# Kernel optimization log

Hardware: AMD Instinct MI355X
Metric: run time of the kernel (lower is better)

Reference implementation:

```python
import jax, jax.numpy as jnp
import numpy as np
import math

D_MODEL = 2048
N_HEADS = 16
HEAD_DIM = 128
ROPE_THETA = 10000.0


def apply_rope(x, pos, theta=ROPE_THETA):
    # x: [b, h, s, d], pos: [b, s] int
    d = x.shape[-1]
    inv_freq = 1.0 / (theta ** (jnp.arange(0, d, 2, dtype=jnp.float32) / d))  # [d/2]
    ang = pos.astype(jnp.float32)[:, None, :, None] * inv_freq  # [b,1,s,d/2]
    cos, sin = jnp.cos(ang), jnp.sin(ang)
    x1, x2 = x[..., 0::2], x[..., 1::2]
    out_even = x1 * cos - x2 * sin
    out_odd = x1 * sin + x2 * cos
    return jnp.stack([out_even, out_odd], axis=-1).reshape(x.shape)


def setup_inputs() -> dict:
    key = jax.random.key(0)
    ks = jax.random.split(key, 5)
    b, s = 2, 2048
    scale = 1.0 / math.sqrt(D_MODEL)
    x = jax.random.normal(ks[0], (b, s, D_MODEL), dtype=jnp.float32)
    Wq = jax.random.normal(ks[1], (D_MODEL, D_MODEL), dtype=jnp.float32) * scale
    Wk = jax.random.normal(ks[2], (D_MODEL, D_MODEL), dtype=jnp.float32) * scale
    Wv = jax.random.normal(ks[3], (D_MODEL, D_MODEL), dtype=jnp.float32) * scale
    Wo = jax.random.normal(ks[4], (D_MODEL, D_MODEL), dtype=jnp.float32) * scale
    token_positions = jnp.broadcast_to(jnp.arange(s, dtype=jnp.int32), (b, s))
    return {"x": x, "token_positions": token_positions, "Wq": Wq, "Wk": Wk, "Wv": Wv, "Wo": Wo}


def reference(x, token_positions, Wq, Wk, Wv, Wo):
    b, s, _ = x.shape
    h, d = N_HEADS, HEAD_DIM
    # QKV projections (Linear: x @ W.T), split heads: b s (h d) -> b h s d
    def proj(W):
        y = jnp.einsum('bse,fe->bsf', x, W)
        return y.reshape(b, s, h, d).transpose(0, 2, 1, 3)
    Q, K, V = proj(Wq), proj(Wk), proj(Wv)
    Q = apply_rope(Q, token_positions)
    K = apply_rope(K, token_positions)
    logits = jnp.einsum('bhqd,bhkd->bhqk', Q, K) / math.sqrt(d)
    causal = jnp.triu(jnp.ones((s, s), dtype=bool), 1)
    logits = jnp.where(causal, -jnp.inf, logits)
    attn = jax.nn.softmax(logits, axis=-1)
    ctx = jnp.einsum('bhqk,bhkd->bhqd', attn, V)
    ctx = ctx.transpose(0, 2, 1, 3).reshape(b, s, h * d)
    return jnp.einsum('bsf,ef->bse', ctx, Wo)
```

## Files before the change

### kernel.cpp

```cpp
#include <hip/hip_runtime.h>
#include <cstdint>
#include <cstddef>

typedef __bf16 bf16_t;
typedef __bf16 bf16x8 __attribute__((ext_vector_type(8)));
typedef float  f32x4  __attribute__((ext_vector_type(4)));

#define SEQ 2048
#define NH  16
#define HD  128
#define MM  4096
#define KK  2048

#define ASYNC16(g, l) __builtin_amdgcn_global_load_lds( \
    (const __attribute__((address_space(1))) void*)(g), \
    (__attribute__((address_space(3))) void*)(l), 16, 0, 0)

__global__ __launch_bounds__(256) void cast_all(const float* __restrict__ x,
                                                const float* __restrict__ Wq,
                                                const float* __restrict__ Wk,
                                                const float* __restrict__ Wv,
                                                const float* __restrict__ Wo,
                                                bf16_t* __restrict__ xb,
                                                bf16_t* __restrict__ wqkv,
                                                bf16_t* __restrict__ wob) {
    int i = blockIdx.x * 256 + threadIdx.x;
    const float* src;
    bf16_t* dst;
    int off;
    if (i < 2097152) { src = x; dst = xb; off = i; }
    else {
        int j = i - 2097152;
        int sel = j >> 20; off = j & 0xFFFFF;
        if (sel < 3) { src = (sel == 0) ? Wq : (sel == 1) ? Wk : Wv; dst = wqkv + (size_t)sel * 4194304; }
        else         { src = Wo; dst = wob; }
    }
    float4 v = ((const float4*)src)[off];
    union { bf16_t h[4]; uint2 u; } t;
    t.h[0] = (bf16_t)v.x; t.h[1] = (bf16_t)v.y;
    t.h[2] = (bf16_t)v.z; t.h[3] = (bf16_t)v.w;
    ((uint2*)dst)[off] = t.u;
}

union SMemU {
    struct { bf16_t A[2][4096]; bf16_t B[2][4096]; } st;
    bf16_t epi[64 * 136];
};

template<int MODE>
__device__ __forceinline__ void gemm_body(SMemU& sm,
                                          const bf16_t* __restrict__ A,
                                          const bf16_t* __restrict__ B,
                                          void* __restrict__ Cout,
                                          bf16_t* __restrict__ Kout,
                                          bf16_t* __restrict__ Vout,
                                          const int* __restrict__ pos) {
    const int tid = threadIdx.x;
    const int w = tid >> 6, l = tid & 63;
    const int lane16 = l & 15, quad = l >> 4;
    const int tm = blockIdx.y, tn = blockIdx.x;
    const int wm = w >> 1, wn = w & 1;

    const bf16_t* pA0 = A + (size_t)(tm * 128 + (2 * w + 0) * 16 + lane16) * KK + quad * 8;
    const bf16_t* pA1 = A + (size_t)(tm * 128 + (2 * w + 1) * 16 + lane16) * KK + quad * 8;
    const bf16_t* pB0 = B + (size_t)(tn * 128 + (2 * w + 0) * 16 + lane16) * KK + quad * 8;
    const bf16_t* pB1 = B + (size_t)(tn * 128 + (2 * w + 1) * 16 + lane16) * KK + quad * 8;

    bf16_t* wA0_0 = &sm.st.A[0][(2 * w + 0) * 512];
    bf16_t* wA1_0 = &sm.st.A[0][(2 * w + 1) * 512];
    bf16_t* wA0_1 = &sm.st.A[1][(2 * w + 0) * 512];
    bf16_t* wA1_1 = &sm.st.A[1][(2 * w + 1) * 512];
    bf16_t* wB0_0 = &sm.st.B[0][(2 * w + 0) * 512];
    bf16_t* wB1_0 = &sm.st.B[0][(2 * w + 1) * 512];
    bf16_t* wB0_1 = &sm.st.B[1][(2 * w + 0) * 512];
    bf16_t* wB1_1 = &sm.st.B[1][(2 * w + 1) * 512];

    f32x4 acc[4][4];
    for (int i = 0; i < 4; i++)
        for (int j = 0; j < 4; j++) acc[i][j] = (f32x4){0.f, 0.f, 0.f, 0.f};

    for (int k0 = 0; k0 < KK; k0 += 64) {
        __syncthreads();
        ASYNC16(pA0, wA0_0); ASYNC16(pA1, wA1_0);
        ASYNC16(pB0, wB0_0); ASYNC16(pB1, wB1_0);
        ASYNC16(pA0 + 32, wA0_1); ASYNC16(pA1 + 32, wA1_1);
        ASYNC16(pB0 + 32, wB0_1); ASYNC16(pB1 + 32, wB1_1);
        pA0 += 64; pA1 += 64; pB0 += 64; pB1 += 64;
        __syncthreads();
        #pragma unroll
        for (int kh = 0; kh < 2; kh++) {
            const bf16_t* rA = &sm.st.A[kh][wm * 2048 + l * 8];
            const bf16_t* rB = &sm.st.B[kh][wn * 2048 + l * 8];
            bf16x8 af[4], bfr[4];
            for (int i = 0; i < 4; i++) af[i]  = *(const bf16x8*)(rA + i * 512);
            for (int j = 0; j < 4; j++) bfr[j] = *(const bf16x8*)(rB + j * 512);
            for (int i = 0; i < 4; i++)
                for (int j = 0; j < 4; j++)
                    acc[i][j] = __builtin_amdgcn_mfma_f32_16x16x32_bf16(af[i], bfr[j], acc[i][j], 0, 0, 0);
        }
    }

    if (MODE == 1) {
        const int mbase = tm * 128 + wm * 64;
        const int nbase = tn * 128 + wn * 64;
        for (int i = 0; i < 4; i++)
            for (int j = 0; j < 4; j++) {
                const int n  = nbase + j * 16 + lane16;
                const int m0 = mbase + i * 16 + quad * 4;
                for (int r = 0; r < 4; r++)
                    ((float*)Cout)[(size_t)(m0 + r) * 2048 + n] = acc[i][j][r];
            }
        return;
    }

    const int mbase = tm * 128;
    const int nb    = tn * 128;
    const int sel   = nb >> 11;
    const int hh    = (nb & 2047) >> 7;
    const int bidx  = mbase >> 11;
    const int g  = tid >> 4;
    const int c8 = (tid & 15) * 8;

    if (sel < 2) {
        bf16_t* dstbase = ((sel == 0) ? (bf16_t*)Cout : Kout) +
                          (size_t)(bidx * NH + hh) * SEQ * HD;
        const float qs = (sel == 0) ? 0.08838834764831845f : 1.0f;
        for (int half = 0; half < 2; half++) {
            __syncthreads();
            if (wm == half) {
                for (int i = 0; i < 4; i++)
                    for (int j = 0; j < 4; j++)
                        for (int r = 0; r < 4; r++)
                            sm.epi[(i * 16 + quad * 4 + r) * 136 + wn * 64 + j * 16 + lane16] =
                                (bf16_t)acc[i][j][r];
            }
            __syncthreads();
            for (int p = 0; p < 4; p++) {
                const int rid = p * 16 + g;
                const int s = (mbase & 2047) + half * 64 + rid;
                bf16x8 v = *(const bf16x8*)&sm.epi[rid * 136 + c8];
                const float pp = (float)pos[bidx * SEQ + s];
                union { bf16_t h8[8]; uint4 u; } o;
                for (int t = 0; t < 4; t++) {
                    const int fi = (c8 >> 1) + t;
                    const float freq = exp2f(-(float)fi * 0.20762050593045857f);
                    const float ang = pp * freq;
                    const float sn = __sinf(ang), cs = __cosf(ang);
                    const float x1 = (float)v[2 * t], x2 = (float)v[2 * t + 1];
                    o.h8[2 * t]     = (bf16_t)((x1 * cs - x2 * sn) * qs);
                    o.h8[2 * t + 1] = (bf16_t)((x1 * sn + x2 * cs) * qs);
                }
                *(uint4*)(dstbase + (size_t)s * HD + c8) = o.u;
            }
        }
    } else {
        bf16_t* dstb = Vout + (size_t)(bidx * NH + hh) * HD * SEQ;
        const int s0 = mbase & 2047;
        for (int half = 0; half < 2; half++) {
            __syncthreads();
            if (wn == half) {
                for (int i = 0; i < 4; i++)
                    for (int j = 0; j < 4; j++) {
                        union { bf16_t h4[4]; uint2 u; } pk;
                        for (int r = 0; r < 4; r++) pk.h4[r] = (bf16_t)acc[i][j][r];
                        *(uint2*)&sm.epi[(j * 16 + lane16) * 136 + wm * 64 + i * 16 + quad * 4] = pk.u;
                    }
            }
            __syncthreads();
            for (int p = 0; p < 4; p++) {
                const int rid = p * 16 + g;
                const int d = half * 64 + rid;
                bf16x8 v = *(const bf16x8*)&sm.epi[rid * 136 + c8];
                *(uint4*)(dstb + (size_t)d * SEQ + s0 + c8) = *(const uint4*)&v;
            }
        }
    }
}

__global__ __launch_bounds__(256) void gemm_qkv(const bf16_t* __restrict__ A,
                                                const bf16_t* __restrict__ B,
                                                bf16_t* __restrict__ Qout,
                                                bf16_t* __restrict__ Kout,
                                                bf16_t* __restrict__ Vout,
                                                const int* __restrict__ pos) {
    __shared__ SMemU sm;
    gemm_body<3>(sm, A, B, (void*)Qout, Kout, Vout, pos);
}

__global__ __launch_bounds__(256) void gemm_out(const bf16_t* __restrict__ A,
                                                const bf16_t* __restrict__ B,
                                                float* __restrict__ Cout) {
    __shared__ SMemU sm;
    gemm_body<1>(sm, A, B, (void*)Cout, nullptr, nullptr, nullptr);
}

__global__ __launch_bounds__(256) void attn_kernel(const bf16_t* __restrict__ Q,
                                                   const bf16_t* __restrict__ K,
                                                   const bf16_t* __restrict__ Vt,
                                                   bf16_t* __restrict__ ctx) {
    const int flat = blockIdx.x;
    const int bh = flat & 31;
    const int bt = flat >> 5;
    const int h = bh & 15, b = bh >> 4;
    const bf16_t* Qh = Q  + (size_t)bh * SEQ * HD;
    const bf16_t* Kh = K  + (size_t)bh * SEQ * HD;
    const bf16_t* Vh = Vt + (size_t)bh * HD * SEQ;

    const int tid = threadIdx.x;
    const int w = tid >> 6, l = tid & 63;
    const int lane16 = l & 15, quad = l >> 4;

    __shared__ bf16_t kt[2][16 * 512];
    __shared__ bf16_t vt[2][16 * 512];
    __shared__ bf16_t pbuf[4][1024];

    for (int half = 0; half < 2; half++) {
        const int qt = half ? (31 - bt) : bt;
        const int q0 = qt * 64 + w * 16;

        bf16x8 qf[4];
        {
            const bf16_t* qrow = Qh + (size_t)(q0 + lane16) * HD + quad * 8;
            for (int kc = 0; kc < 4; kc++) qf[kc] = *(const bf16x8*)(qrow + kc * 32);
        }

        f32x4 o[8];
        for (int dt = 0; dt < 8; dt++) o[dt] = (f32x4){0.f, 0.f, 0.f, 0.f};
        float m_s = -INFINITY, l_s = 0.f;

        __syncthreads();
        for (int ii = 0; ii < 4; ii++) {
            const int f = w * 4 + ii;
            const int nt = f >> 2, kc = f & 3;
            ASYNC16(Kh + (size_t)(nt * 16 + lane16) * HD + kc * 32 + quad * 8, &kt[0][f * 512]);
            const int dt = f >> 1, kk = f & 1;
            ASYNC16(Vh + (size_t)(dt * 16 + lane16) * SEQ + kk * 32 + quad * 8, &vt[0][f * 512]);
        }

        int cur = 0;
        for (int kb = 0; kb <= qt; kb++) {
            const int k0 = kb * 64;
            __syncthreads();
            if (kb < qt) {
                const int kn = k0 + 64;
                for (int ii = 0; ii < 4; ii++) {
                    const int f = w * 4 + ii;
                    const int nt = f >> 2, kc = f & 3;
                    ASYNC16(Kh + (size_t)(kn + nt * 16 + lane16) * HD + kc * 32 + quad * 8,
                            &kt[1 - cur][f * 512]);
                    const int dt = f >> 1, kk = f & 1;
                    ASYNC16(Vh + (size_t)(dt * 16 + lane16) * SEQ + kn + kk * 32 + quad * 8,
                            &vt[1 - cur][f * 512]);
                }
            }
            const bf16_t* ktc = kt[cur];
            const bf16_t* vtc = vt[cur];

            f32x4 sacc[4];
            for (int nt = 0; nt < 4; nt++) sacc[nt] = (f32x4){0.f, 0.f, 0.f, 0.f};
            for (int nt = 0; nt < 4; nt++)
                for (int kc = 0; kc < 4; kc++) {
                    bf16x8 kf = *(const bf16x8*)&ktc[(nt * 4 + kc) * 512 + l * 8];
                    sacc[nt] = __builtin_amdgcn_mfma_f32_16x16x32_bf16(kf, qf[kc], sacc[nt], 0, 0, 0);
                }
            if (kb == qt) {
                const int qg = q0 + lane16;
                for (int nt = 0; nt < 4; nt++)
                    for (int r = 0; r < 4; r++) {
                        const int kg = k0 + nt * 16 + quad * 4 + r;
                        if (kg > qg) sacc[nt][r] = -INFINITY;
                    }
            }
            float rowmax = sacc[0][0];
            for (int nt = 0; nt < 4; nt++)
                for (int r = 0; r < 4; r++) rowmax = fmaxf(rowmax, sacc[nt][r]);
            rowmax = fmaxf(rowmax, __shfl_xor(rowmax, 16, 64));
            rowmax = fmaxf(rowmax, __shfl_xor(rowmax, 32, 64));
            const float mnew = fmaxf(m_s, rowmax);
            const float a = __expf(m_s - mnew);
            m_s = mnew;
            float ssum = 0.f;
            for (int nt = 0; nt < 4; nt++) {
                union { bf16_t h4[4]; uint2 u; } pk;
                for (int r = 0; r < 4; r++) {
                    const float e = __expf(sacc[nt][r] - mnew);
                    ssum += e;
                    pk.h4[r] = (bf16_t)e;
                }
                const int addr = (nt >> 1) * 512 +
                                 (((nt & 1) * 2 + (quad >> 1)) * 16 + lane16) * 8 +
                                 (quad & 1) * 4;
                *(uint2*)&pbuf[w][addr] = pk.u;
            }
            ssum += __shfl_xor(ssum, 16, 64);
            ssum += __shfl_xor(ssum, 32, 64);
            l_s = l_s * a + ssum;

            float ar[4];
            for (int r = 0; r < 4; r++) ar[r] = __shfl(a, (quad << 2) | r, 16);
            for (int dt = 0; dt < 8; dt++)
                for (int r = 0; r < 4; r++) o[dt][r] *= ar[r];
            for (int kk = 0; kk < 2; kk++) {
                bf16x8 pf = *(const bf16x8*)&pbuf[w][kk * 512 + l * 8];
                for (int dt = 0; dt < 8; dt++) {
                    bf16x8 vf = *(const bf16x8*)&vtc[(dt * 2 + kk) * 512 + l * 8];
                    o[dt] = __builtin_amdgcn_mfma_f32_16x16x32_bf16(pf, vf, o[dt], 0, 0, 0);
                }
            }
            cur ^= 1;
        }

        float inv[4];
        for (int r = 0; r < 4; r++) inv[r] = 1.0f / __shfl(l_s, (quad << 2) | r, 16);
        for (int r = 0; r < 4; r++) {
            const int qg = q0 + quad * 4 + r;
            bf16_t* dst = ctx + ((size_t)(b * SEQ + qg)) * (NH * HD) + h * HD;
            for (int dt = 0; dt < 8; dt++)
                dst[dt * 16 + lane16] = (bf16_t)(o[dt][r] * inv[r]);
        }
        __syncthreads();
    }
}

extern "C" void kernel_launch(void* const* d_in, const int* in_sizes, int n_in,
                              void* d_out, int out_size, void* d_ws, size_t ws_size,
                              hipStream_t stream) {
    const float* x  = (const float*)d_in[0];
    const int* pos  = (const int*)d_in[1];
    const float* Wq = (const float*)d_in[2];
    const float* Wk = (const float*)d_in[3];
    const float* Wv = (const float*)d_in[4];
    const float* Wo = (const float*)d_in[5];

    char* ws = (char*)d_ws;
    bf16_t* xb   = (bf16_t*)(ws);
    bf16_t* wqkv = (bf16_t*)(ws + (16u << 20));
    bf16_t* wob  = (bf16_t*)(ws + (40u << 20));
    bf16_t* Qb   = (bf16_t*)(ws + (48u << 20));
    bf16_t* Kb   = (bf16_t*)(ws + (64u << 20));
    bf16_t* Vt   = (bf16_t*)(ws + (80u << 20));
    bf16_t* ctx  = (bf16_t*)(ws + (96u << 20));

    cast_all<<<24576, 256, 0, stream>>>(x, Wq, Wk, Wv, Wo, xb, wqkv, wob);

    dim3 gq(6144 / 128, MM / 128);
    gemm_qkv<<<gq, 256, 0, stream>>>(xb, wqkv, Qb, Kb, Vt, pos);

    attn_kernel<<<512, 256, 0, stream>>>(Qb, Kb, Vt, ctx);

    dim3 gg(2048 / 128, MM / 128);
    gemm_out<<<gg, 256, 0, stream>>>(ctx, wob, (float*)d_out);
}
```

Baseline: 462.3 us.

## Double-buffer GEMM K-loop with async LDS prefetch of next tile

Restructures the projection GEMM main loop to issue async global-to-LDS loads for the next 32-wide K slice into the alternate buffer, then compute MFMAs on the current one. Previously each iteration loaded both halves of a 64-wide slice and waited before computing, so memory and math never overlapped. The loop now runs one barrier per 32-wide step, the same barrier count per K element as before. The gain depends on whether the compiler puts a full vmcnt wait before the LDS reads, which would serialize the prefetch again.

```diff
diff --git a/kernel.cpp b/kernel.cpp
--- a/kernel.cpp
+++ b/kernel.cpp
@@ -66,38 +66,35 @@
     const bf16_t* pB0 = B + (size_t)(tn * 128 + (2 * w + 0) * 16 + lane16) * KK + quad * 8;
     const bf16_t* pB1 = B + (size_t)(tn * 128 + (2 * w + 1) * 16 + lane16) * KK + quad * 8;
 
-    bf16_t* wA0_0 = &sm.st.A[0][(2 * w + 0) * 512];
-    bf16_t* wA1_0 = &sm.st.A[0][(2 * w + 1) * 512];
-    bf16_t* wA0_1 = &sm.st.A[1][(2 * w + 0) * 512];
-    bf16_t* wA1_1 = &sm.st.A[1][(2 * w + 1) * 512];
-    bf16_t* wB0_0 = &sm.st.B[0][(2 * w + 0) * 512];
-    bf16_t* wB1_0 = &sm.st.B[0][(2 * w + 1) * 512];
-    bf16_t* wB0_1 = &sm.st.B[1][(2 * w + 0) * 512];
-    bf16_t* wB1_1 = &sm.st.B[1][(2 * w + 1) * 512];
-
     f32x4 acc[4][4];
     for (int i = 0; i < 4; i++)
         for (int j = 0; j < 4; j++) acc[i][j] = (f32x4){0.f, 0.f, 0.f, 0.f};
 
-    for (int k0 = 0; k0 < KK; k0 += 64) {
+    ASYNC16(pA0, &sm.st.A[0][(2 * w + 0) * 512]);
+    ASYNC16(pA1, &sm.st.A[0][(2 * w + 1) * 512]);
+    ASYNC16(pB0, &sm.st.B[0][(2 * w + 0) * 512]);
+    ASYNC16(pB1, &sm.st.B[0][(2 * w + 1) * 512]);
+
+    int cur = 0;
+    for (int k0 = 0; k0 < KK; k0 += 32) {
         __syncthreads();
-        ASYNC16(pA0, wA0_0); ASYNC16(pA1, wA1_0);
-        ASYNC16(pB0, wB0_0); ASYNC16(pB1, wB1_0);
-        ASYNC16(pA0 + 32, wA0_1); ASYNC16(pA1 + 32, wA1_1);
-        ASYNC16(pB0 + 32, wB0_1); ASYNC16(pB1 + 32, wB1_1);
-        pA0 += 64; pA1 += 64; pB0 += 64; pB1 += 64;
-        __syncthreads();
-        #pragma unroll
-        for (int kh = 0; kh < 2; kh++) {
-            const bf16_t* rA = &sm.st.A[kh][wm * 2048 + l * 8];
-            const bf16_t* rB = &sm.st.B[kh][wn * 2048 + l * 8];
-            bf16x8 af[4], bfr[4];
-            for (int i = 0; i < 4; i++) af[i]  = *(const bf16x8*)(rA + i * 512);
-            for (int j = 0; j < 4; j++) bfr[j] = *(const bf16x8*)(rB + j * 512);
-            for (int i = 0; i < 4; i++)
-                for (int j = 0; j < 4; j++)
-                    acc[i][j] = __builtin_amdgcn_mfma_f32_16x16x32_bf16(af[i], bfr[j], acc[i][j], 0, 0, 0);
-        }
+        if (k0 + 32 < KK) {
+            const int nbuf = 1 - cur;
+            ASYNC16(pA0 + 32, &sm.st.A[nbuf][(2 * w + 0) * 512]);
+            ASYNC16(pA1 + 32, &sm.st.A[nbuf][(2 * w + 1) * 512]);
+            ASYNC16(pB0 + 32, &sm.st.B[nbuf][(2 * w + 0) * 512]);
+            ASYNC16(pB1 + 32, &sm.st.B[nbuf][(2 * w + 1) * 512]);
+            pA0 += 32; pA1 += 32; pB0 += 32; pB1 += 32;
+        }
+        const bf16_t* rA = &sm.st.A[cur][wm * 2048 + l * 8];
+        const bf16_t* rB = &sm.st.B[cur][wn * 2048 + l * 8];
+        bf16x8 af[4], bfr[4];
+        for (int i = 0; i < 4; i++) af[i]  = *(const bf16x8*)(rA + i * 512);
+        for (int j = 0; j < 4; j++) bfr[j] = *(const bf16x8*)(rB + j * 512);
+        for (int i = 0; i < 4; i++)
+            for (int j = 0; j < 4; j++)
+                acc[i][j] = __builtin_amdgcn_mfma_f32_16x16x32_bf16(af[i], bfr[j], acc[i][j], 0, 0, 0);
+        cur ^= 1;
     }
 
     if (MODE == 1) {
```

After: 460.6 us. Within noise of the previous version (-0.4%).
